# Kernel tuning notes

Measured on AMD Instinct MI355X. Metric: run time of the kernel, lower is better.

The kernel has to match this reference:

```python
import jax, jax.numpy as jnp
import numpy as np

B, N, E, DM, DN, H = 8, 128, 2, 128, 128, 4
NEG = -1000000.0


def setup_inputs() -> dict:
    key = jax.random.key(0)
    k1, k2, k3, k4 = jax.random.split(key, 4)
    edge_msgs = jax.random.normal(k1, (B, N, N, E, DM), dtype=jnp.float32)
    node_states = jax.random.normal(k2, (B, N, DN), dtype=jnp.float32)
    edges = jax.random.randint(k3, (B, N, N, E + 1), 0, 2).astype(jnp.int32)
    # Dense(1) kernel per head over concat([edge_msgs, node_states]) -> [H, DM+DN]
    W = jax.random.normal(k4, (H, DM + DN), dtype=jnp.float32) * 0.05
    b = jnp.zeros((H,), dtype=jnp.float32)
    return {"edge_msgs": edge_msgs, "node_states": node_states, "W": W, "b": b, "edges": edges}


def reference(edge_msgs, node_states, W, b, edges):
    Dm = edge_msgs.shape[-1]
    W_msg, W_node = W[:, :Dm], W[:, Dm:]
    # Fused equivalent of tile+concat+Dense(1): split the kernel.
    # s: [B, sender, recv, etype, head]
    s = jnp.einsum('bsrec,hc->bsreh', edge_msgs, W_msg)
    s = s + jnp.einsum('brc,hc->brh', node_states, W_node)[:, None, :, None, :]
    s = jax.nn.elu(s + b)
    # mask: edges[...,1:] is 0/1 over [B,N,N,E]; 0 -> -1e6 bias
    bias = (1.0 - edges[..., 1:].astype(s.dtype)) * NEG  # [B,N,N,E]
    weights = jax.nn.softmax(s + bias[..., None], axis=1)  # softmax over senders
    # weighted sum over senders and edge types, per head: [B, recv, head, Dm]
    out = jnp.einsum('bsreh,bsrec->brhc', weights, edge_msgs)
    Bq, Nq = out.shape[:2]
    return out.reshape(Bq, Nq, -1)  # heads concatenated along last axis
```

## Files before the change

### kernel.cpp

```cpp
#include <hip/hip_runtime.h>
#include <math.h>

#define NB 8
#define NN 128
static constexpr float NEGV = -1000000.0f;

__global__ __launch_bounds__(512)
void edge_attn_kernel(const float* __restrict__ edge_msgs,
                      const float* __restrict__ node_states,
                      const float* __restrict__ W,
                      const float* __restrict__ bvec,
                      const int*   __restrict__ edges,
                      float* __restrict__ out) {
    const int blk = blockIdx.x;
    const int b = blk >> 7;
    const int r = blk & 127;

    const int t  = threadIdx.x;
    const int w  = t >> 6;
    const int l  = t & 63;
    const int e  = l >> 5;
    const int c4 = l & 31;

    __shared__ float part[128 * 68];
    __shared__ float wts [2 * 128 * 5];
    __shared__ float ebias[128 * 2];
    __shared__ float nodep[4];
    __shared__ float outbuf[8][4][128];

    float4 wm0 = *(const float4*)(W +   0 + c4 * 4);
    float4 wm1 = *(const float4*)(W + 256 + c4 * 4);
    float4 wm2 = *(const float4*)(W + 512 + c4 * 4);
    float4 wm3 = *(const float4*)(W + 768 + c4 * 4);

    const float* bp = edge_msgs
        + (size_t)b * (NN * NN * 256)
        + (size_t)r * 256
        + e * 128 + c4 * 4;

    float4 V0, V1, V2, V3, V4, V5, V6, V7, V8, V9, V10, V11, V12, V13, V14, V15;

#define LOADV(i) V##i = *(const float4*)(bp + (size_t)(w + 8 * (i)) * 32768);
    LOADV(0)  LOADV(1)  LOADV(2)  LOADV(3)
    LOADV(4)  LOADV(5)  LOADV(6)  LOADV(7)
    LOADV(8)  LOADV(9)  LOADV(10) LOADV(11)
    LOADV(12) LOADV(13) LOADV(14) LOADV(15)
#undef LOADV

    if (w == 0) {
        float2 nv  = *(const float2*)(node_states + ((size_t)b * NN + r) * 128 + l * 2);
        float2 wn0 = *(const float2*)(W + 128 + l * 2);
        float2 wn1 = *(const float2*)(W + 384 + l * 2);
        float2 wn2 = *(const float2*)(W + 640 + l * 2);
        float2 wn3 = *(const float2*)(W + 896 + l * 2);
        float np0 = nv.x * wn0.x + nv.y * wn0.y;
        float np1 = nv.x * wn1.x + nv.y * wn1.y;
        float np2 = nv.x * wn2.x + nv.y * wn2.y;
        float np3 = nv.x * wn3.x + nv.y * wn3.y;
        #pragma unroll
        for (int m = 32; m >= 1; m >>= 1) {
            np0 += __shfl_xor(np0, m);
            np1 += __shfl_xor(np1, m);
            np2 += __shfl_xor(np2, m);
            np3 += __shfl_xor(np3, m);
        }
        if (l == 0) { nodep[0] = np0; nodep[1] = np1; nodep[2] = np2; nodep[3] = np3; }
    }

    if (t < 256) {
        int s  = t >> 1;
        int ec = t & 1;
        int ev = edges[(((size_t)b * NN + s) * NN + r) * 3 + 1 + ec];
        ebias[s * 2 + ec] = (1.0f - (float)ev) * NEGV;
    }

    const int hsel = l & 3;
    const int g    = (l >> 2) & 7;
    const bool o1  = (l & 1) != 0;
    const bool o2  = (l & 2) != 0;

#define SCOREV(d, si) {                                                        \
    float p0 = d.x * wm0.x + d.y * wm0.y + d.z * wm0.z + d.w * wm0.w;          \
    float p1 = d.x * wm1.x + d.y * wm1.y + d.z * wm1.z + d.w * wm1.w;          \
    float p2 = d.x * wm2.x + d.y * wm2.y + d.z * wm2.z + d.w * wm2.w;          \
    float p3 = d.x * wm3.x + d.y * wm3.y + d.z * wm3.z + d.w * wm3.w;          \
    float x01 = o1 ? p1 : p0, y01 = o1 ? p0 : p1;                              \
    float x23 = o1 ? p3 : p2, y23 = o1 ? p2 : p3;                              \
    float r01 = x01 + __shfl_xor(y01, 1);                                      \
    float r23 = x23 + __shfl_xor(y23, 1);                                      \
    float x2 = o2 ? r23 : r01, y2 = o2 ? r01 : r23;                            \
    float val = x2 + __shfl_xor(y2, 2);                                        \
    part[(w + 8 * (si)) * 68 + e * 32 + hsel * 8 + g] = val;                   \
}
    SCOREV(V0, 0)   SCOREV(V1, 1)   SCOREV(V2, 2)   SCOREV(V3, 3)
    SCOREV(V4, 4)   SCOREV(V5, 5)   SCOREV(V6, 6)   SCOREV(V7, 7)
    SCOREV(V8, 8)   SCOREV(V9, 9)   SCOREV(V10, 10) SCOREV(V11, 11)
    SCOREV(V12, 12) SCOREV(V13, 13) SCOREV(V14, 14) SCOREV(V15, 15)
#undef SCOREV
    __syncthreads();

    if (t < 256) {
        int p  = t >> 5;
        int j  = t & 31;
        int es = p & 1;
        int h  = p >> 1;
        float bb = bvec[h] + nodep[h];
        float y0, y1, y2, y3;
        #define SCORE(k, dst)                                                  \
        {                                                                      \
            int s = j + 32 * k;                                                \
            const float* q = &part[s * 68 + es * 32 + h * 8];                  \
            float4 qa = *(const float4*)q;                                     \
            float4 qb = *(const float4*)(q + 4);                               \
            float x = (qa.x + qa.y + qa.z + qa.w)                              \
                    + (qb.x + qb.y + qb.z + qb.w) + bb;                        \
            x = x > 0.f ? x : expm1f(x);                                       \
            dst = x + ebias[s * 2 + es];                                       \
        }
        SCORE(0, y0) SCORE(1, y1) SCORE(2, y2) SCORE(3, y3)
        #undef SCORE
        float m4 = fmaxf(fmaxf(y0, y1), fmaxf(y2, y3));
        #pragma unroll
        for (int m = 16; m >= 1; m >>= 1) m4 = fmaxf(m4, __shfl_xor(m4, m));
        y0 = __expf(y0 - m4); y1 = __expf(y1 - m4);
        y2 = __expf(y2 - m4); y3 = __expf(y3 - m4);
        float sum = y0 + y1 + y2 + y3;
        #pragma unroll
        for (int m = 16; m >= 1; m >>= 1) sum += __shfl_xor(sum, m);
        float inv = 1.0f / sum;
        wts[es * 640 + (j +  0) * 5 + h] = y0 * inv;
        wts[es * 640 + (j + 32) * 5 + h] = y1 * inv;
        wts[es * 640 + (j + 64) * 5 + h] = y2 * inv;
        wts[es * 640 + (j + 96) * 5 + h] = y3 * inv;
    }
    __syncthreads();

    float4 a0 = {0,0,0,0}, a1 = {0,0,0,0}, a2 = {0,0,0,0}, a3 = {0,0,0,0};
#define AGGV(d, si) {                                                          \
    int s = w + 8 * (si);                                                      \
    float w0 = wts[e * 640 + s * 5 + 0];                                       \
    float w1 = wts[e * 640 + s * 5 + 1];                                       \
    float w2 = wts[e * 640 + s * 5 + 2];                                       \
    float w3 = wts[e * 640 + s * 5 + 3];                                       \
    a0.x += w0 * d.x; a0.y += w0 * d.y; a0.z += w0 * d.z; a0.w += w0 * d.w;    \
    a1.x += w1 * d.x; a1.y += w1 * d.y; a1.z += w1 * d.z; a1.w += w1 * d.w;    \
    a2.x += w2 * d.x; a2.y += w2 * d.y; a2.z += w2 * d.z; a2.w += w2 * d.w;    \
    a3.x += w3 * d.x; a3.y += w3 * d.y; a3.z += w3 * d.z; a3.w += w3 * d.w;    \
}
    AGGV(V0, 0)   AGGV(V1, 1)   AGGV(V2, 2)   AGGV(V3, 3)
    AGGV(V4, 4)   AGGV(V5, 5)   AGGV(V6, 6)   AGGV(V7, 7)
    AGGV(V8, 8)   AGGV(V9, 9)   AGGV(V10, 10) AGGV(V11, 11)
    AGGV(V12, 12) AGGV(V13, 13) AGGV(V14, 14) AGGV(V15, 15)
#undef AGGV

    a0.x += __shfl_xor(a0.x, 32); a0.y += __shfl_xor(a0.y, 32); a0.z += __shfl_xor(a0.z, 32); a0.w += __shfl_xor(a0.w, 32);
    a1.x += __shfl_xor(a1.x, 32); a1.y += __shfl_xor(a1.y, 32); a1.z += __shfl_xor(a1.z, 32); a1.w += __shfl_xor(a1.w, 32);
    a2.x += __shfl_xor(a2.x, 32); a2.y += __shfl_xor(a2.y, 32); a2.z += __shfl_xor(a2.z, 32); a2.w += __shfl_xor(a2.w, 32);
    a3.x += __shfl_xor(a3.x, 32); a3.y += __shfl_xor(a3.y, 32); a3.z += __shfl_xor(a3.z, 32); a3.w += __shfl_xor(a3.w, 32);

    if (e == 0) {
        *(float4*)&outbuf[w][0][c4 * 4] = a0;
        *(float4*)&outbuf[w][1][c4 * 4] = a1;
        *(float4*)&outbuf[w][2][c4 * 4] = a2;
        *(float4*)&outbuf[w][3][c4 * 4] = a3;
    }
    __syncthreads();

    {
        int h = t >> 7;
        int c = t & 127;
        float sv = 0.f;
        #pragma unroll
        for (int k = 0; k < 8; ++k) sv += outbuf[k][h][c];
        out[((size_t)b * NN + r) * 512 + t] = sv;
    }
}

extern "C" void kernel_launch(void* const* d_in, const int* in_sizes, int n_in,
                              void* d_out, int out_size, void* d_ws, size_t ws_size,
                              hipStream_t stream) {
    const float* edge_msgs   = (const float*)d_in[0];
    const float* node_states = (const float*)d_in[1];
    const float* W           = (const float*)d_in[2];
    const float* bvec        = (const float*)d_in[3];
    const int*   edges       = (const int*)d_in[4];
    float* out = (float*)d_out;

    dim3 grid(NB * NN);
    dim3 block(512);
    edge_attn_kernel<<<grid, block, 0, stream>>>(edge_msgs, node_states, W, bvec, edges, out);
}
```

Measured before the change: 32.15 us.

## Split sender softmax into two halves with flash-style partial combine kernel

Splits each (batch, receiver) block into two 256-thread blocks that each handle half of the senders. Each block writes unnormalized weighted sums plus per-half max and sum-exp to workspace, and a second kernel merges them with online-softmax rescaling. The goal is more, smaller blocks for better occupancy and latency hiding. The cost is an extra launch and about 8 MB of workspace traffic for the partial outputs.

```diff
diff --git a/kernel.cpp b/kernel.cpp
--- a/kernel.cpp
+++ b/kernel.cpp
@@ -5,16 +5,19 @@
 #define NN 128
 static constexpr float NEGV = -1000000.0f;
 
-__global__ __launch_bounds__(512)
-void edge_attn_kernel(const float* __restrict__ edge_msgs,
-                      const float* __restrict__ node_states,
-                      const float* __restrict__ W,
-                      const float* __restrict__ bvec,
-                      const int*   __restrict__ edges,
-                      float* __restrict__ out) {
-    const int blk = blockIdx.x;
-    const int b = blk >> 7;
-    const int r = blk & 127;
+__global__ __launch_bounds__(256)
+void edge_attn_partial(const float* __restrict__ edge_msgs,
+                       const float* __restrict__ node_states,
+                       const float* __restrict__ W,
+                       const float* __restrict__ bvec,
+                       const int*   __restrict__ edges,
+                       float* __restrict__ pout,
+                       float* __restrict__ mlm,
+                       float* __restrict__ mll) {
+    const int blk  = blockIdx.x;
+    const int r    = blk & 127;
+    const int half = (blk >> 7) & 1;
+    const int b    = blk >> 8;
 
     const int t  = threadIdx.x;
     const int w  = t >> 6;
@@ -22,11 +25,11 @@
     const int e  = l >> 5;
     const int c4 = l & 31;
 
-    __shared__ float part[128 * 68];
-    __shared__ float wts [2 * 128 * 5];
-    __shared__ float ebias[128 * 2];
+    __shared__ float part[64 * 68];
+    __shared__ float wts [2 * 64 * 5];
+    __shared__ float ebias[64 * 2];
     __shared__ float nodep[4];
-    __shared__ float outbuf[8][4][128];
+    __shared__ float outbuf[4][2][4][128];
 
     float4 wm0 = *(const float4*)(W +   0 + c4 * 4);
     float4 wm1 = *(const float4*)(W + 256 + c4 * 4);
@@ -35,12 +38,13 @@
 
     const float* bp = edge_msgs
         + (size_t)b * (NN * NN * 256)
+        + (size_t)(half * 64) * 32768
         + (size_t)r * 256
         + e * 128 + c4 * 4;
 
     float4 V0, V1, V2, V3, V4, V5, V6, V7, V8, V9, V10, V11, V12, V13, V14, V15;
 
-#define LOADV(i) V##i = *(const float4*)(bp + (size_t)(w + 8 * (i)) * 32768);
+#define LOADV(i) V##i = *(const float4*)(bp + (size_t)(w + 4 * (i)) * 32768);
     LOADV(0)  LOADV(1)  LOADV(2)  LOADV(3)
     LOADV(4)  LOADV(5)  LOADV(6)  LOADV(7)
     LOADV(8)  LOADV(9)  LOADV(10) LOADV(11)
@@ -67,11 +71,12 @@
         if (l == 0) { nodep[0] = np0; nodep[1] = np1; nodep[2] = np2; nodep[3] = np3; }
     }
 
-    if (t < 256) {
-        int s  = t >> 1;
-        int ec = t & 1;
+    if (t < 128) {
+        int s_loc = t >> 1;
+        int ec    = t & 1;
+        int s     = half * 64 + s_loc;
         int ev = edges[(((size_t)b * NN + s) * NN + r) * 3 + 1 + ec];
-        ebias[s * 2 + ec] = (1.0f - (float)ev) * NEGV;
+        ebias[s_loc * 2 + ec] = (1.0f - (float)ev) * NEGV;
     }
 
     const int hsel = l & 3;
@@ -90,7 +95,7 @@
     float r23 = x23 + __shfl_xor(y23, 1);                                      \
     float x2 = o2 ? r23 : r01, y2 = o2 ? r01 : r23;                            \
     float val = x2 + __shfl_xor(y2, 2);                                        \
-    part[(w + 8 * (si)) * 68 + e * 32 + hsel * 8 + g] = val;                   \
+    part[(w + 4 * (si)) * 68 + e * 32 + hsel * 8 + g] = val;                   \
 }
     SCOREV(V0, 0)   SCOREV(V1, 1)   SCOREV(V2, 2)   SCOREV(V3, 3)
     SCOREV(V4, 4)   SCOREV(V5, 5)   SCOREV(V6, 6)   SCOREV(V7, 7)
@@ -99,49 +104,51 @@
 #undef SCOREV
     __syncthreads();
 
-    if (t < 256) {
+    {
         int p  = t >> 5;
         int j  = t & 31;
         int es = p & 1;
         int h  = p >> 1;
         float bb = bvec[h] + nodep[h];
-        float y0, y1, y2, y3;
+        float y0, y1;
         #define SCORE(k, dst)                                                  \
         {                                                                      \
-            int s = j + 32 * k;                                                \
-            const float* q = &part[s * 68 + es * 32 + h * 8];                  \
+            int s_loc = j + 32 * k;                                            \
+            const float* q = &part[s_loc * 68 + es * 32 + h * 8];              \
             float4 qa = *(const float4*)q;                                     \
             float4 qb = *(const float4*)(q + 4);                               \
             float x = (qa.x + qa.y + qa.z + qa.w)                              \
                     + (qb.x + qb.y + qb.z + qb.w) + bb;                        \
             x = x > 0.f ? x : expm1f(x);                                       \
-            dst = x + ebias[s * 2 + es];                                       \
+            dst = x + ebias[s_loc * 2 + es];                                   \
         }
-        SCORE(0, y0) SCORE(1, y1) SCORE(2, y2) SCORE(3, y3)
+        SCORE(0, y0) SCORE(1, y1)
         #undef SCORE
-        float m4 = fmaxf(fmaxf(y0, y1), fmaxf(y2, y3));
+        float m2 = fmaxf(y0, y1);
         #pragma unroll
-        for (int m = 16; m >= 1; m >>= 1) m4 = fmaxf(m4, __shfl_xor(m4, m));
-        y0 = __expf(y0 - m4); y1 = __expf(y1 - m4);
-        y2 = __expf(y2 - m4); y3 = __expf(y3 - m4);
-        float sum = y0 + y1 + y2 + y3;
+        for (int m = 16; m >= 1; m >>= 1) m2 = fmaxf(m2, __shfl_xor(m2, m));
+        float p0 = __expf(y0 - m2);
+        float p1 = __expf(y1 - m2);
+        float ls = p0 + p1;
         #pragma unroll
-        for (int m = 16; m >= 1; m >>= 1) sum += __shfl_xor(sum, m);
-        float inv = 1.0f / sum;
-        wts[es * 640 + (j +  0) * 5 + h] = y0 * inv;
-        wts[es * 640 + (j + 32) * 5 + h] = y1 * inv;
-        wts[es * 640 + (j + 64) * 5 + h] = y2 * inv;
-        wts[es * 640 + (j + 96) * 5 + h] = y3 * inv;
+        for (int m = 16; m >= 1; m >>= 1) ls += __shfl_xor(ls, m);
+        wts[es * 320 + (j +  0) * 5 + h] = p0;
+        wts[es * 320 + (j + 32) * 5 + h] = p1;
+        if (j == 0) {
+            size_t mli = ((((size_t)half * NB + b) * NN + r) * 2 + es) * 4 + h;
+            mlm[mli] = m2;
+            mll[mli] = ls;
+        }
     }
     __syncthreads();
 
     float4 a0 = {0,0,0,0}, a1 = {0,0,0,0}, a2 = {0,0,0,0}, a3 = {0,0,0,0};
 #define AGGV(d, si) {                                                          \
-    int s = w + 8 * (si);                                                      \
-    float w0 = wts[e * 640 + s * 5 + 0];                                       \
-    float w1 = wts[e * 640 + s * 5 + 1];                                       \
-    float w2 = wts[e * 640 + s * 5 + 2];                                       \
-    float w3 = wts[e * 640 + s * 5 + 3];                                       \
+    int s_loc = w + 4 * (si);                                                  \
+    float w0 = wts[e * 320 + s_loc * 5 + 0];                                   \
+    float w1 = wts[e * 320 + s_loc * 5 + 1];                                   \
+    float w2 = wts[e * 320 + s_loc * 5 + 2];                                   \
+    float w3 = wts[e * 320 + s_loc * 5 + 3];                                   \
     a0.x += w0 * d.x; a0.y += w0 * d.y; a0.z += w0 * d.z; a0.w += w0 * d.w;    \
     a1.x += w1 * d.x; a1.y += w1 * d.y; a1.z += w1 * d.z; a1.w += w1 * d.w;    \
     a2.x += w2 * d.x; a2.y += w2 * d.y; a2.z += w2 * d.z; a2.w += w2 * d.w;    \
@@ -153,27 +160,56 @@
     AGGV(V12, 12) AGGV(V13, 13) AGGV(V14, 14) AGGV(V15, 15)
 #undef AGGV
 
-    a0.x += __shfl_xor(a0.x, 32); a0.y += __shfl_xor(a0.y, 32); a0.z += __shfl_xor(a0.z, 32); a0.w += __shfl_xor(a0.w, 32);
-    a1.x += __shfl_xor(a1.x, 32); a1.y += __shfl_xor(a1.y, 32); a1.z += __shfl_xor(a1.z, 32); a1.w += __shfl_xor(a1.w, 32);
-    a2.x += __shfl_xor(a2.x, 32); a2.y += __shfl_xor(a2.y, 32); a2.z += __shfl_xor(a2.z, 32); a2.w += __shfl_xor(a2.w, 32);
-    a3.x += __shfl_xor(a3.x, 32); a3.y += __shfl_xor(a3.y, 32); a3.z += __shfl_xor(a3.z, 32); a3.w += __shfl_xor(a3.w, 32);
-
-    if (e == 0) {
-        *(float4*)&outbuf[w][0][c4 * 4] = a0;
-        *(float4*)&outbuf[w][1][c4 * 4] = a1;
-        *(float4*)&outbuf[w][2][c4 * 4] = a2;
-        *(float4*)&outbuf[w][3][c4 * 4] = a3;
-    }
+    *(float4*)&outbuf[w][e][0][c4 * 4] = a0;
+    *(float4*)&outbuf[w][e][1][c4 * 4] = a1;
+    *(float4*)&outbuf[w][e][2][c4 * 4] = a2;
+    *(float4*)&outbuf[w][e][3][c4 * 4] = a3;
     __syncthreads();
 
-    {
-        int h = t >> 7;
-        int c = t & 127;
-        float sv = 0.f;
-        #pragma unroll
-        for (int k = 0; k < 8; ++k) sv += outbuf[k][h][c];
-        out[((size_t)b * NN + r) * 512 + t] = sv;
-    }
+    #pragma unroll
+    for (int k = 0; k < 4; ++k) {
+        int idx = t + 256 * k;
+        int ee = idx >> 9;
+        int hh = (idx >> 7) & 3;
+        int cc = idx & 127;
+        float sv = outbuf[0][ee][hh][cc] + outbuf[1][ee][hh][cc]
+                 + outbuf[2][ee][hh][cc] + outbuf[3][ee][hh][cc];
+        size_t po = (((((size_t)half * NB + b) * NN + r) * 2 + ee) * 4 + hh) * 128 + cc;
+        pout[po] = sv;
+    }
+}
+
+__global__ __launch_bounds__(256)
+void edge_attn_combine(const float* __restrict__ pout,
+                       const float* __restrict__ mlm,
+                       const float* __restrict__ mll,
+                       float* __restrict__ out) {
+    int i = blockIdx.x * 256 + threadIdx.x;
+    int c4 = i & 31;
+    int h  = (i >> 5) & 3;
+    int r  = (i >> 7) & 127;
+    int b  = i >> 14;
+
+    const float4* p4 = (const float4*)pout;
+    float4 res = {0, 0, 0, 0};
+    #pragma unroll
+    for (int e = 0; e < 2; ++e) {
+        size_t idx0 = ((((size_t)0 * NB + b) * NN + r) * 2 + e) * 4 + h;
+        size_t idx1 = idx0 + (size_t)NB * NN * 2 * 4;
+        float m0 = mlm[idx0], m1 = mlm[idx1];
+        float l0 = mll[idx0], l1 = mll[idx1];
+        float M  = fmaxf(m0, m1);
+        float w0 = __expf(m0 - M);
+        float w1 = __expf(m1 - M);
+        float inv = 1.0f / (l0 * w0 + l1 * w1);
+        float4 q0 = p4[idx0 * 32 + c4];
+        float4 q1 = p4[idx1 * 32 + c4];
+        res.x += (q0.x * w0 + q1.x * w1) * inv;
+        res.y += (q0.y * w0 + q1.y * w1) * inv;
+        res.z += (q0.z * w0 + q1.z * w1) * inv;
+        res.w += (q0.w * w0 + q1.w * w1) * inv;
+    }
+    ((float4*)out)[i] = res;
 }
 
 extern "C" void kernel_launch(void* const* d_in, const int* in_sizes, int n_in,
@@ -186,7 +222,12 @@
     const int*   edges       = (const int*)d_in[4];
     float* out = (float*)d_out;
 
-    dim3 grid(NB * NN);
-    dim3 block(512);
-    edge_attn_kernel<<<grid, block, 0, stream>>>(edge_msgs, node_states, W, bvec, edges, out);
-}
+    float* pout = (float*)d_ws;
+    float* mlm  = pout + 2097152;
+    float* mll  = mlm + 16384;
+
+    edge_attn_partial<<<dim3(NB * 2 * NN), dim3(256), 0, stream>>>(
+        edge_msgs, node_states, W, bvec, edges, pout, mlm, mll);
+    edge_attn_combine<<<dim3(131072 / 256), dim3(256), 0, stream>>>(
+        pout, mlm, mll, out);
+}
```

Measured after the change: 35.61 us. +10.8%, slower.

## Process two adjacent receivers per 1024-thread block with contiguous 2KB loads

Applied to the files above, without the earlier changes.

Each block now handles two adjacent receiver columns using 16 waves, so every sender row is read as a contiguous 2KB span covering both receivers instead of a separate 1KB span per block. Shared score and softmax buffers are reused serially per receiver, and the output staging buffer aliases the part array. This aims to improve DRAM access contiguity and halve the number of blocks. In exchange it adds extra barriers, halves the grid to 512 blocks, and forces 1024-thread blocks, which may limit occupancy and latency hiding.

```diff
diff --git a/kernel.cpp b/kernel.cpp
--- a/kernel.cpp
+++ b/kernel.cpp
@@ -5,7 +5,7 @@
 #define NN 128
 static constexpr float NEGV = -1000000.0f;
 
-__global__ __launch_bounds__(512)
+__global__ __launch_bounds__(1024)
 void edge_attn_kernel(const float* __restrict__ edge_msgs,
                       const float* __restrict__ node_states,
                       const float* __restrict__ W,
@@ -13,8 +13,9 @@
                       const int*   __restrict__ edges,
                       float* __restrict__ out) {
     const int blk = blockIdx.x;
-    const int b = blk >> 7;
-    const int r = blk & 127;
+    const int rp  = blk & 63;
+    const int b   = blk >> 6;
+    const int r0  = rp * 2;
 
     const int t  = threadIdx.x;
     const int w  = t >> 6;
@@ -23,10 +24,10 @@
     const int c4 = l & 31;
 
     __shared__ float part[128 * 68];
-    __shared__ float wts [2 * 128 * 5];
-    __shared__ float ebias[128 * 2];
-    __shared__ float nodep[4];
-    __shared__ float outbuf[8][4][128];
+    __shared__ float wts [2][2 * 128 * 5];
+    __shared__ float ebias[2][128 * 2];
+    __shared__ float nodep[2][4];
+    float (*outbuf)[4][128] = (float (*)[4][128])part;
 
     float4 wm0 = *(const float4*)(W +   0 + c4 * 4);
     float4 wm1 = *(const float4*)(W + 256 + c4 * 4);
@@ -35,20 +36,22 @@
 
     const float* bp = edge_msgs
         + (size_t)b * (NN * NN * 256)
-        + (size_t)r * 256
+        + (size_t)r0 * 256
         + e * 128 + c4 * 4;
 
-    float4 V0, V1, V2, V3, V4, V5, V6, V7, V8, V9, V10, V11, V12, V13, V14, V15;
-
-#define LOADV(i) V##i = *(const float4*)(bp + (size_t)(w + 8 * (i)) * 32768);
-    LOADV(0)  LOADV(1)  LOADV(2)  LOADV(3)
-    LOADV(4)  LOADV(5)  LOADV(6)  LOADV(7)
-    LOADV(8)  LOADV(9)  LOADV(10) LOADV(11)
-    LOADV(12) LOADV(13) LOADV(14) LOADV(15)
-#undef LOADV
-
-    if (w == 0) {
-        float2 nv  = *(const float2*)(node_states + ((size_t)b * NN + r) * 128 + l * 2);
+    float4 P0, P1, P2, P3, P4, P5, P6, P7;
+    float4 Q0, Q1, Q2, Q3, Q4, Q5, Q6, Q7;
+
+#define LOADP(i)                                                               \
+    P##i = *(const float4*)(bp + (size_t)(w + 16 * (i)) * 32768);              \
+    Q##i = *(const float4*)(bp + (size_t)(w + 16 * (i)) * 32768 + 256);
+    LOADP(0) LOADP(1) LOADP(2) LOADP(3)
+    LOADP(4) LOADP(5) LOADP(6) LOADP(7)
+#undef LOADP
+
+    if (w < 2) {
+        int rr = w;
+        float2 nv  = *(const float2*)(node_states + ((size_t)b * NN + r0 + rr) * 128 + l * 2);
         float2 wn0 = *(const float2*)(W + 128 + l * 2);
         float2 wn1 = *(const float2*)(W + 384 + l * 2);
         float2 wn2 = *(const float2*)(W + 640 + l * 2);
@@ -64,14 +67,15 @@
             np2 += __shfl_xor(np2, m);
             np3 += __shfl_xor(np3, m);
         }
-        if (l == 0) { nodep[0] = np0; nodep[1] = np1; nodep[2] = np2; nodep[3] = np3; }
+        if (l == 0) { nodep[rr][0] = np0; nodep[rr][1] = np1; nodep[rr][2] = np2; nodep[rr][3] = np3; }
     }
 
-    if (t < 256) {
-        int s  = t >> 1;
+    if (t < 512) {
+        int s  = t >> 2;
+        int rr = (t >> 1) & 1;
         int ec = t & 1;
-        int ev = edges[(((size_t)b * NN + s) * NN + r) * 3 + 1 + ec];
-        ebias[s * 2 + ec] = (1.0f - (float)ev) * NEGV;
+        int ev = edges[(((size_t)b * NN + s) * NN + (r0 + rr)) * 3 + 1 + ec];
+        ebias[rr][s * 2 + ec] = (1.0f - (float)ev) * NEGV;
     }
 
     const int hsel = l & 3;
@@ -90,90 +94,112 @@
     float r23 = x23 + __shfl_xor(y23, 1);                                      \
     float x2 = o2 ? r23 : r01, y2 = o2 ? r01 : r23;                            \
     float val = x2 + __shfl_xor(y2, 2);                                        \
-    part[(w + 8 * (si)) * 68 + e * 32 + hsel * 8 + g] = val;                   \
-}
-    SCOREV(V0, 0)   SCOREV(V1, 1)   SCOREV(V2, 2)   SCOREV(V3, 3)
-    SCOREV(V4, 4)   SCOREV(V5, 5)   SCOREV(V6, 6)   SCOREV(V7, 7)
-    SCOREV(V8, 8)   SCOREV(V9, 9)   SCOREV(V10, 10) SCOREV(V11, 11)
-    SCOREV(V12, 12) SCOREV(V13, 13) SCOREV(V14, 14) SCOREV(V15, 15)
+    part[(w + 16 * (si)) * 68 + e * 32 + hsel * 8 + g] = val;                  \
+}
+
+#define SMAX(rr) if (t < 256) {                                                \
+    int p  = t >> 5;                                                           \
+    int j  = t & 31;                                                           \
+    int es = p & 1;                                                            \
+    int h  = p >> 1;                                                           \
+    float bb = bvec[h] + nodep[rr][h];                                         \
+    float y0, y1, y2, y3;                                                      \
+    {                                                                          \
+        float x; const float* q;                                               \
+        q = &part[(j +  0) * 68 + es * 32 + h * 8];                            \
+        { float4 qa = *(const float4*)q, qb = *(const float4*)(q + 4);         \
+          x = qa.x+qa.y+qa.z+qa.w + qb.x+qb.y+qb.z+qb.w + bb;                  \
+          x = x > 0.f ? x : expm1f(x); y0 = x + ebias[rr][(j+ 0)*2+es]; }      \
+        q = &part[(j + 32) * 68 + es * 32 + h * 8];                            \
+        { float4 qa = *(const float4*)q, qb = *(const float4*)(q + 4);         \
+          x = qa.x+qa.y+qa.z+qa.w + qb.x+qb.y+qb.z+qb.w + bb;                  \
+          x = x > 0.f ? x : expm1f(x); y1 = x + ebias[rr][(j+32)*2+es]; }      \
+        q = &part[(j + 64) * 68 + es * 32 + h * 8];                            \
+        { float4 qa = *(const float4*)q, qb = *(const float4*)(q + 4);         \
+          x = qa.x+qa.y+qa.z+qa.w + qb.x+qb.y+qb.z+qb.w + bb;                  \
+          x = x > 0.f ? x : expm1f(x); y2 = x + ebias[rr][(j+64)*2+es]; }      \
+        q = &part[(j + 96) * 68 + es * 32 + h * 8];                            \
+        { float4 qa = *(const float4*)q, qb = *(const float4*)(q + 4);         \
+          x = qa.x+qa.y+qa.z+qa.w + qb.x+qb.y+qb.z+qb.w + bb;                  \
+          x = x > 0.f ? x : expm1f(x); y3 = x + ebias[rr][(j+96)*2+es]; }      \
+    }                                                                          \
+    float m4 = fmaxf(fmaxf(y0, y1), fmaxf(y2, y3));                            \
+    _Pragma("unroll")                                                          \
+    for (int m = 16; m >= 1; m >>= 1) m4 = fmaxf(m4, __shfl_xor(m4, m));       \
+    y0 = __expf(y0 - m4); y1 = __expf(y1 - m4);                                \
+    y2 = __expf(y2 - m4); y3 = __expf(y3 - m4);                                \
+    float sum = y0 + y1 + y2 + y3;                                             \
+    _Pragma("unroll")                                                          \
+    for (int m = 16; m >= 1; m >>= 1) sum += __shfl_xor(sum, m);               \
+    float inv = 1.0f / sum;                                                    \
+    wts[rr][es * 640 + (j +  0) * 5 + h] = y0 * inv;                           \
+    wts[rr][es * 640 + (j + 32) * 5 + h] = y1 * inv;                           \
+    wts[rr][es * 640 + (j + 64) * 5 + h] = y2 * inv;                           \
+    wts[rr][es * 640 + (j + 96) * 5 + h] = y3 * inv;                           \
+}
+
+    SCOREV(P0, 0) SCOREV(P1, 1) SCOREV(P2, 2) SCOREV(P3, 3)
+    SCOREV(P4, 4) SCOREV(P5, 5) SCOREV(P6, 6) SCOREV(P7, 7)
+    __syncthreads();
+    SMAX(0)
+    __syncthreads();
+    SCOREV(Q0, 0) SCOREV(Q1, 1) SCOREV(Q2, 2) SCOREV(Q3, 3)
+    SCOREV(Q4, 4) SCOREV(Q5, 5) SCOREV(Q6, 6) SCOREV(Q7, 7)
+    __syncthreads();
+    SMAX(1)
+    __syncthreads();
 #undef SCOREV
-    __syncthreads();
-
-    if (t < 256) {
-        int p  = t >> 5;
-        int j  = t & 31;
-        int es = p & 1;
-        int h  = p >> 1;
-        float bb = bvec[h] + nodep[h];
-        float y0, y1, y2, y3;
-        #define SCORE(k, dst)                                                  \
-        {                                                                      \
-            int s = j + 32 * k;                                                \
-            const float* q = &part[s * 68 + es * 32 + h * 8];                  \
-            float4 qa = *(const float4*)q;                                     \
-            float4 qb = *(const float4*)(q + 4);                               \
-            float x = (qa.x + qa.y + qa.z + qa.w)                              \
-                    + (qb.x + qb.y + qb.z + qb.w) + bb;                        \
-            x = x > 0.f ? x : expm1f(x);                                       \
-            dst = x + ebias[s * 2 + es];                                       \
-        }
-        SCORE(0, y0) SCORE(1, y1) SCORE(2, y2) SCORE(3, y3)
-        #undef SCORE
-        float m4 = fmaxf(fmaxf(y0, y1), fmaxf(y2, y3));
-        #pragma unroll
-        for (int m = 16; m >= 1; m >>= 1) m4 = fmaxf(m4, __shfl_xor(m4, m));
-        y0 = __expf(y0 - m4); y1 = __expf(y1 - m4);
-        y2 = __expf(y2 - m4); y3 = __expf(y3 - m4);
-        float sum = y0 + y1 + y2 + y3;
-        #pragma unroll
-        for (int m = 16; m >= 1; m >>= 1) sum += __shfl_xor(sum, m);
-        float inv = 1.0f / sum;
-        wts[es * 640 + (j +  0) * 5 + h] = y0 * inv;
-        wts[es * 640 + (j + 32) * 5 + h] = y1 * inv;
-        wts[es * 640 + (j + 64) * 5 + h] = y2 * inv;
-        wts[es * 640 + (j + 96) * 5 + h] = y3 * inv;
-    }
-    __syncthreads();
-
-    float4 a0 = {0,0,0,0}, a1 = {0,0,0,0}, a2 = {0,0,0,0}, a3 = {0,0,0,0};
-#define AGGV(d, si) {                                                          \
-    int s = w + 8 * (si);                                                      \
-    float w0 = wts[e * 640 + s * 5 + 0];                                       \
-    float w1 = wts[e * 640 + s * 5 + 1];                                       \
-    float w2 = wts[e * 640 + s * 5 + 2];                                       \
-    float w3 = wts[e * 640 + s * 5 + 3];                                       \
+#undef SMAX
+
+#define AGGV(d, si, rr) {                                                      \
+    int s = w + 16 * (si);                                                     \
+    float w0 = wts[rr][e * 640 + s * 5 + 0];                                   \
+    float w1 = wts[rr][e * 640 + s * 5 + 1];                                   \
+    float w2 = wts[rr][e * 640 + s * 5 + 2];                                   \
+    float w3 = wts[rr][e * 640 + s * 5 + 3];                                   \
     a0.x += w0 * d.x; a0.y += w0 * d.y; a0.z += w0 * d.z; a0.w += w0 * d.w;    \
     a1.x += w1 * d.x; a1.y += w1 * d.y; a1.z += w1 * d.z; a1.w += w1 * d.w;    \
     a2.x += w2 * d.x; a2.y += w2 * d.y; a2.z += w2 * d.z; a2.w += w2 * d.w;    \
     a3.x += w3 * d.x; a3.y += w3 * d.y; a3.z += w3 * d.z; a3.w += w3 * d.w;    \
 }
-    AGGV(V0, 0)   AGGV(V1, 1)   AGGV(V2, 2)   AGGV(V3, 3)
-    AGGV(V4, 4)   AGGV(V5, 5)   AGGV(V6, 6)   AGGV(V7, 7)
-    AGGV(V8, 8)   AGGV(V9, 9)   AGGV(V10, 10) AGGV(V11, 11)
-    AGGV(V12, 12) AGGV(V13, 13) AGGV(V14, 14) AGGV(V15, 15)
+
+#define AGGPHASE(PFX, rr)                                                      \
+    {                                                                          \
+        float4 a0 = {0,0,0,0}, a1 = {0,0,0,0}, a2 = {0,0,0,0}, a3 = {0,0,0,0}; \
+        AGGV(PFX##0, 0, rr) AGGV(PFX##1, 1, rr)                                \
+        AGGV(PFX##2, 2, rr) AGGV(PFX##3, 3, rr)                                \
+        AGGV(PFX##4, 4, rr) AGGV(PFX##5, 5, rr)                                \
+        AGGV(PFX##6, 6, rr) AGGV(PFX##7, 7, rr)                                \
+        a0.x += __shfl_xor(a0.x, 32); a0.y += __shfl_xor(a0.y, 32);            \
+        a0.z += __shfl_xor(a0.z, 32); a0.w += __shfl_xor(a0.w, 32);            \
+        a1.x += __shfl_xor(a1.x, 32); a1.y += __shfl_xor(a1.y, 32);            \
+        a1.z += __shfl_xor(a1.z, 32); a1.w += __shfl_xor(a1.w, 32);            \
+        a2.x += __shfl_xor(a2.x, 32); a2.y += __shfl_xor(a2.y, 32);            \
+        a2.z += __shfl_xor(a2.z, 32); a2.w += __shfl_xor(a2.w, 32);            \
+        a3.x += __shfl_xor(a3.x, 32); a3.y += __shfl_xor(a3.y, 32);            \
+        a3.z += __shfl_xor(a3.z, 32); a3.w += __shfl_xor(a3.w, 32);            \
+        if (e == 0) {                                                          \
+            *(float4*)&outbuf[w][0][c4 * 4] = a0;                              \
+            *(float4*)&outbuf[w][1][c4 * 4] = a1;                              \
+            *(float4*)&outbuf[w][2][c4 * 4] = a2;                              \
+            *(float4*)&outbuf[w][3][c4 * 4] = a3;                              \
+        }                                                                      \
+    }                                                                          \
+    __syncthreads();                                                           \
+    if (t < 512) {                                                             \
+        int h = t >> 7;                                                        \
+        int c = t & 127;                                                       \
+        float sv = 0.f;                                                        \
+        _Pragma("unroll")                                                      \
+        for (int k = 0; k < 16; ++k) sv += outbuf[k][h][c];                    \
+        out[((size_t)b * NN + (r0 + rr)) * 512 + t] = sv;                      \
+    }                                                                          \
+    __syncthreads();
+
+    AGGPHASE(P, 0)
+    AGGPHASE(Q, 1)
+#undef AGGPHASE
 #undef AGGV
-
-    a0.x += __shfl_xor(a0.x, 32); a0.y += __shfl_xor(a0.y, 32); a0.z += __shfl_xor(a0.z, 32); a0.w += __shfl_xor(a0.w, 32);
-    a1.x += __shfl_xor(a1.x, 32); a1.y += __shfl_xor(a1.y, 32); a1.z += __shfl_xor(a1.z, 32); a1.w += __shfl_xor(a1.w, 32);
-    a2.x += __shfl_xor(a2.x, 32); a2.y += __shfl_xor(a2.y, 32); a2.z += __shfl_xor(a2.z, 32); a2.w += __shfl_xor(a2.w, 32);
-    a3.x += __shfl_xor(a3.x, 32); a3.y += __shfl_xor(a3.y, 32); a3.z += __shfl_xor(a3.z, 32); a3.w += __shfl_xor(a3.w, 32);
-
-    if (e == 0) {
-        *(float4*)&outbuf[w][0][c4 * 4] = a0;
-        *(float4*)&outbuf[w][1][c4 * 4] = a1;
-        *(float4*)&outbuf[w][2][c4 * 4] = a2;
-        *(float4*)&outbuf[w][3][c4 * 4] = a3;
-    }
-    __syncthreads();
-
-    {
-        int h = t >> 7;
-        int c = t & 127;
-        float sv = 0.f;
-        #pragma unroll
-        for (int k = 0; k < 8; ++k) sv += outbuf[k][h][c];
-        out[((size_t)b * NN + r) * 512 + t] = sv;
-    }
 }
 
 extern "C" void kernel_launch(void* const* d_in, const int* in_sizes, int n_in,
@@ -186,7 +212,7 @@
     const int*   edges       = (const int*)d_in[4];
     float* out = (float*)d_out;
 
-    dim3 grid(NB * NN);
-    dim3 block(512);
+    dim3 grid(NB * (NN / 2));
+    dim3 block(1024);
     edge_attn_kernel<<<grid, block, 0, stream>>>(edge_msgs, node_states, W, bvec, edges, out);
 }
```

Result: slower. 43.06 us (+33.9%).
